# Kernel optimization log

Measured on AMD Instinct MI355X. Metric: run time of the kernel, lower is better.

The kernel has to match this reference:

```python
import jax, jax.numpy as jnp
import numpy as np

N = 16384   # nodes = batch(4) * 64*64 grid
E = 32768   # edges per edge set
L = 32      # LATENT_DIMS
D = 2       # DEPTH (message-passing layers per GNOBlock)
KD = 64     # KERNEL_DIMS
TIN = 10    # TIME_STEPS_IN

def gelu(x):
    return jax.nn.gelu(x, approximate=False)  # torch F.gelu default (erf)

def setup_inputs() -> dict:
    key = jax.random.key(0)
    ks = iter(jax.random.split(key, 64))
    def nrm(shape, s=0.1):
        return jax.random.normal(next(ks), shape, dtype=jnp.float32) * s
    def ridx():
        return jax.random.randint(next(ks), (2, E), 0, N)
    inp = {
        'nodes': nrm((N, TIN), 1.0),
        'grid': jax.random.uniform(next(ks), (N, 2), dtype=jnp.float32),
    }
    for nm in ['11', '12', '22', '23', '33', '32', '21']:
        inp[f'edge_index_{nm}'] = ridx()
    for nm in ['11', '12', '22', '23', '33', '32', '21']:
        inp[f'edge_attr_{nm}'] = nrm((E, 5), 1.0)
    inp['batch_size'] = 4
    inp['image_size'] = 64
    # projector MLP: in_dims=TIN+2 -> hidden L//2 -> L
    inp['proj_w1'] = nrm((TIN + 2, L // 2)); inp['proj_b1'] = jnp.zeros((L // 2,), jnp.float32)
    inp['proj_w2'] = nrm((L // 2, L));       inp['proj_b2'] = jnp.zeros((L,), jnp.float32)
    # decoder MLP: L -> L//2 -> 1
    inp['dec_w1'] = nrm((L, L // 2)); inp['dec_b1'] = jnp.zeros((L // 2,), jnp.float32)
    inp['dec_w2'] = nrm((L // 2, 1)); inp['dec_b2'] = jnp.zeros((1,), jnp.float32)
    # 7 GNOBlocks x D layers: edge kernel MLP (5 -> KD -> L*L) + node linear (L -> L)
    inp['kw1'] = nrm((7, D, 5, KD));      inp['kb1'] = jnp.zeros((7, D, KD), jnp.float32)
    inp['kw2'] = nrm((7, D, KD, L * L));  inp['kb2'] = jnp.zeros((7, D, L * L), jnp.float32)
    inp['lw'] = nrm((7, D, L, L));        inp['lb'] = jnp.zeros((7, D, L), jnp.float32)
    return inp

def _mlp(x, w1, b1, w2, b2):
    return gelu(x @ w1 + b1) @ w2 + b2

def _gno_block(i, x, eidx, eattr, kw1, kb1, kw2, kb2, lw, lb):
    src, dst = eidx[0], eidx[1]
    n = x.shape[0]
    deg = jax.ops.segment_sum(jnp.ones_like(dst, x.dtype), dst, num_segments=n)
    inv_deg = jnp.where(deg > 0, 1.0 / jnp.maximum(deg, 1.0), 0.0)[:, None]
    for d in range(kw1.shape[1]):
        # edge-conditioned kernel: [E, L, L]
        k = _mlp(eattr, kw1[i, d], kb1[i, d], kw2[i, d], kb2[i, d]).reshape(-1, x.shape[1], x.shape[1])
        msg = jnp.einsum('eio,ei->eo', k, x[src])            # gather + per-edge matvec
        agg = jax.ops.segment_sum(msg, dst, num_segments=n) * inv_deg  # scatter-mean
        x = gelu(x @ lw[i, d] + lb[i, d] + agg)              # root linear + activation
    return x

def reference(nodes, grid, edge_index_11, edge_index_12, edge_index_22, edge_index_23,
              edge_index_33, edge_index_32, edge_index_21, edge_attr_11, edge_attr_12,
              edge_attr_22, edge_attr_23, edge_attr_33, edge_attr_32, edge_attr_21,
              batch_size, image_size, proj_w1, proj_b1, proj_w2, proj_b2,
              dec_w1, dec_b1, dec_w2, dec_b2, kw1, kb1, kw2, kb2, lw, lb):
    x = jnp.concatenate([nodes, grid], axis=-1)
    x = gelu(_mlp(x, proj_w1, proj_b1, proj_w2, proj_b2))
    # block param index order matches init order: k11,k22,k33,k12,k23,k32,k21
    n11 = _gno_block(0, x, edge_index_11, edge_attr_11, kw1, kb1, kw2, kb2, lw, lb)
    n12 = _gno_block(3, x, edge_index_12, edge_attr_12, kw1, kb1, kw2, kb2, lw, lb)
    n22 = _gno_block(1, n12, edge_index_22, edge_attr_22, kw1, kb1, kw2, kb2, lw, lb)
    n23 = _gno_block(4, n12, edge_index_23, edge_attr_23, kw1, kb1, kw2, kb2, lw, lb)
    n33 = _gno_block(2, n23, edge_index_33, edge_attr_33, kw1, kb1, kw2, kb2, lw, lb)
    n32 = _gno_block(5, n33, edge_index_32, edge_attr_32, kw1, kb1, kw2, kb2, lw, lb)
    n21 = _gno_block(6, n32 + n22, edge_index_21, edge_attr_21, kw1, kb1, kw2, kb2, lw, lb)
    out = _mlp(n21 + n11, dec_w1, dec_b1, dec_w2, dec_b2)
    return out
```

## Files before the change

kernel.cpp:

```cpp
#include <hip/hip_runtime.h>

#define Nn 16384
#define Ee 32768
#define NL (Nn * 32)

typedef _Float16 hf16;
typedef _Float16 half8 __attribute__((ext_vector_type(8)));
typedef float f32x16 __attribute__((ext_vector_type(16)));

__device__ __forceinline__ float gelu_f(float x) {
    return 0.5f * x * (1.0f + erff(x * 0.7071067811865476f));
}

__device__ __forceinline__ f32x16 zero16() {
    f32x16 v;
#pragma unroll
    for (int r = 0; r < 16; ++r) v[r] = 0.0f;
    return v;
}

struct EPtrs { const int* p[7]; };
struct EA14  { const float* p[14]; };

__global__ __launch_bounds__(256) void proj_kernel(
    const float* __restrict__ nodes, const float* __restrict__ grid2,
    const float* __restrict__ w1, const float* __restrict__ b1,
    const float* __restrict__ w2, const float* __restrict__ b2,
    float* __restrict__ x0, int* __restrict__ deg_i, int* __restrict__ cursor)
{
    const int n = blockIdx.x * 256 + threadIdx.x;
    float in[12];
#pragma unroll
    for (int j = 0; j < 10; ++j) in[j] = nodes[n * 10 + j];
    in[10] = grid2[n * 2 + 0];
    in[11] = grid2[n * 2 + 1];
    float h[16];
#pragma unroll
    for (int j = 0; j < 16; ++j) {
        float a = b1[j];
#pragma unroll
        for (int i = 0; i < 12; ++i) a = fmaf(in[i], w1[i * 16 + j], a);
        h[j] = gelu_f(a);
    }
#pragma unroll
    for (int o = 0; o < 32; ++o) {
        float a = b2[o];
#pragma unroll
        for (int j = 0; j < 16; ++j) a = fmaf(h[j], w2[j * 32 + o], a);
        x0[(size_t)n * 32 + o] = gelu_f(a);
    }
#pragma unroll
    for (int s = 0; s < 7; ++s) { deg_i[s * Nn + n] = 0; cursor[s * Nn + n] = 0; }
}

__global__ __launch_bounds__(256) void count_deg_kernel(EPtrs ei, int* __restrict__ deg_i)
{
    const int t = blockIdx.x * 256 + threadIdx.x;
    const int s = t >> 15;
    const int e = t & (Ee - 1);
    const int dst = ei.p[s][Ee + e];
    atomicAdd(&deg_i[s * Nn + dst], 1);
}

__global__ __launch_bounds__(256) void scan_kernel(const int* __restrict__ deg_i,
                                                   int* __restrict__ off)
{
    const int s = blockIdx.x;
    const int t = threadIdx.x;
    const int* d = deg_i + (size_t)s * Nn;
    int* o = off + (size_t)s * (Nn + 1);
    int local[64];
    int sum = 0;
#pragma unroll
    for (int j = 0; j < 64; ++j) { local[j] = d[t * 64 + j]; sum += local[j]; }
    __shared__ int ps[256];
    ps[t] = sum;
    __syncthreads();
    for (int st = 1; st < 256; st <<= 1) {
        int v = (t >= st) ? ps[t - st] : 0;
        __syncthreads();
        ps[t] += v;
        __syncthreads();
    }
    int base = (t > 0) ? ps[t - 1] : 0;
#pragma unroll
    for (int j = 0; j < 64; ++j) { o[t * 64 + j] = base; base += local[j]; }
    if (t == 255) o[Nn] = base;
}

__global__ __launch_bounds__(256) void rank_kernel(EPtrs ei, const int* __restrict__ off,
                                                   int* __restrict__ cursor,
                                                   int* __restrict__ eord)
{
    const int t = blockIdx.x * 256 + threadIdx.x;
    const int s = t >> 15;
    const int e = t & (Ee - 1);
    const int dst = ei.p[s][Ee + e];
    const int r = off[(size_t)s * (Nn + 1) + dst] + atomicAdd(&cursor[s * Nn + dst], 1);
    eord[(size_t)s * Ee + r] = e;
}

__global__ __launch_bounds__(256) void wprep_kernel(const float* __restrict__ kw2,
                                                    hf16* __restrict__ Wpack)
{
    const int id = blockIdx.x >> 5;
    const int nt = blockIdx.x & 31;
    const int t = threadIdx.x;
    const int ks = t >> 6, lane = t & 63;
    const float* kw2l = kw2 + (size_t)id * 65536;
    half8 vh, vl;
#pragma unroll
    for (int j = 0; j < 8; ++j) {
        const int k = ks * 16 + (lane >> 5) * 8 + j;
        const float v = kw2l[(size_t)k * 1024 + (lane & 31) * 32 + nt];
        const hf16 h = (hf16)v;
        vh[j] = h;
        vl[j] = (hf16)((v - (float)h) * 1024.0f);
    }
    half8* dst = (half8*)(Wpack + ((size_t)(id * 32 + nt) * 8 + ks * 2) * 512);
    dst[0 * 64 + lane] = vh;
    dst[1 * 64 + lane] = vl;
}

__global__ __launch_bounds__(256) void kprep_kernel(const float* __restrict__ kb2,
                                                    float* __restrict__ kb2C)
{
    const int id = blockIdx.x;
    const int t = threadIdx.x;
#pragma unroll
    for (int c = 0; c < 4; ++c) {
        const int ent = t * 4 + c;
        const int nt = ent >> 5;
        const int hi = (ent >> 4) & 1;
        const int r = ent & 15;
        const int i = (r & 3) + 8 * (r >> 2) + 4 * hi;
        kb2C[(size_t)id * 1024 + ent] = kb2[(size_t)id * 1024 + i * 32 + nt];
    }
}

__global__ __launch_bounds__(256) void hprep_kernel(
    EA14 ea, const float* __restrict__ kw1, const float* __restrict__ kb1,
    hf16* __restrict__ Hpack)
{
    const int b = blockIdx.x;
    const int u = b >> 8;
    const int tgrp = b & 255;
    const int t = threadIdx.x, l = t & 63, wv = t >> 6;
    const int tile = tgrp * 4 + wv;
    const int eg = tile * 32 + (l & 31);
    const float* kw1u = kw1 + (size_t)u * 320;
    const float* kb1u = kb1 + (size_t)u * 64;
    float ea5[5];
#pragma unroll
    for (int j = 0; j < 5; ++j) ea5[j] = ea.p[u][(size_t)eg * 5 + j];
    half8* hp = (half8*)Hpack;
#pragma unroll
    for (int ks = 0; ks < 4; ++ks) {
        half8 vh, vl;
#pragma unroll
        for (int j = 0; j < 8; ++j) {
            const int k = ks * 16 + (l >> 5) * 8 + j;
            float pre = kb1u[k];
#pragma unroll
            for (int q = 0; q < 5; ++q) pre = fmaf(ea5[q], kw1u[q * 64 + k], pre);
            const float H = gelu_f(pre);
            const hf16 hv = (hf16)H;
            vh[j] = hv;
            vl[j] = (hf16)((H - (float)hv) * 1024.0f);
        }
        const size_t fb = ((size_t)(u * 1024 + tile) * 8 + ks * 2) * 64;
        hp[fb + l] = vh;
        hp[fb + 64 + l] = vl;
    }
}

__global__ __launch_bounds__(256) void gemm_kernel(
    const float* __restrict__ xa, const float* __restrict__ xb,
    const int* __restrict__ esrc,
    const hf16* __restrict__ HpackU,
    const hf16* __restrict__ WpackL,
    const float* __restrict__ kb2CL,
    float* __restrict__ msgS)
{
    __shared__ __align__(16) hf16 wLDS[2 * 4096];
    half8* wl8 = (half8*)wLDS;

    const int lb = ((blockIdx.x & 7) << 7) + (blockIdx.x >> 3);
    const int eblk = lb >> 2;
    const int qid = lb & 3;
    const int t = threadIdx.x, l = t & 63, wv = t >> 6;
    const int tile = eblk * 4 + wv;

    const half8* hp = (const half8*)HpackU + (size_t)tile * 512;
    half8 Hh[4], Hl[4];
#pragma unroll
    for (int ks = 0; ks < 4; ++ks) {
        Hh[ks] = hp[(ks * 2 + 0) * 64 + l];
        Hl[ks] = hp[(ks * 2 + 1) * 64 + l];
    }

    const int hi = l >> 5;
    const int el = tile * 32 + (l & 31);
    const int src = esrc[el];
    float xsr[16];
#pragma unroll
    for (int c = 0; c < 4; ++c) {
        float4 v = *reinterpret_cast<const float4*>(xa + (size_t)src * 32 + c * 8 + hi * 4);
        if (xb) {
            float4 u = *reinterpret_cast<const float4*>(xb + (size_t)src * 32 + c * 8 + hi * 4);
            v.x += u.x; v.y += u.y; v.z += u.z; v.w += u.w;
        }
        xsr[c * 4 + 0] = v.x; xsr[c * 4 + 1] = v.y;
        xsr[c * 4 + 2] = v.z; xsr[c * 4 + 3] = v.w;
    }

    const half8* wsrc = (const half8*)(WpackL + (size_t)qid * 8 * 4096);
    const float* kbB = kb2CL + hi * 16;

    {
        half8 s0 = wsrc[t * 2 + 0];
        half8 s1 = wsrc[t * 2 + 1];
        wl8[t * 2 + 0] = s0;
        wl8[t * 2 + 1] = s1;
    }
    __syncthreads();

    float4 p4;
    int buf = 0;
#pragma unroll
    for (int nt8 = 0; nt8 < 8; ++nt8) {
        half8 s0, s1;
        if (nt8 < 7) {
            s0 = wsrc[(nt8 + 1) * 512 + t * 2 + 0];
            s1 = wsrc[(nt8 + 1) * 512 + t * 2 + 1];
        }

        half8 WH[4], WL[4];
#pragma unroll
        for (int ks = 0; ks < 4; ++ks) {
            WH[ks] = wl8[buf * 512 + (ks * 2 + 0) * 64 + l];
            WL[ks] = wl8[buf * 512 + (ks * 2 + 1) * 64 + l];
        }

        const int nt = qid * 8 + nt8;
        float kb[16];
#pragma unroll
        for (int c = 0; c < 4; ++c) {
            const float4 kv = *reinterpret_cast<const float4*>(kbB + nt * 32 + c * 4);
            kb[c * 4 + 0] = kv.x; kb[c * 4 + 1] = kv.y;
            kb[c * 4 + 2] = kv.z; kb[c * 4 + 3] = kv.w;
        }

        f32x16 ah = zero16(), ax = zero16();
#pragma unroll
        for (int ks = 0; ks < 4; ++ks) {
            ah = __builtin_amdgcn_mfma_f32_32x32x16_f16(WH[ks], Hh[ks], ah, 0, 0, 0);
            ax = __builtin_amdgcn_mfma_f32_32x32x16_f16(WL[ks], Hh[ks], ax, 0, 0, 0);
            ax = __builtin_amdgcn_mfma_f32_32x32x16_f16(WH[ks], Hl[ks], ax, 0, 0, 0);
        }
        float ph = 0.0f, px = 0.0f, pk = 0.0f;
#pragma unroll
        for (int r = 0; r < 16; ++r) {
            ph = fmaf(ah[r], xsr[r], ph);
            px = fmaf(ax[r], xsr[r], px);
            pk = fmaf(kb[r], xsr[r], pk);
        }
        float p = fmaf(px, 9.765625e-4f, ph) + pk;
        p += __shfl_xor(p, 32);
        p4[nt8 & 3] = p;
        if ((nt8 & 3) == 3 && l < 32)
            *reinterpret_cast<float4*>(msgS + (size_t)el * 32 + qid * 8 + (nt8 - 3)) = p4;

        if (nt8 < 7) {
            wl8[(buf ^ 1) * 512 + t * 2 + 0] = s0;
            wl8[(buf ^ 1) * 512 + t * 2 + 1] = s1;
        }
        __syncthreads();
        buf ^= 1;
    }
}

__global__ __launch_bounds__(256) void node_update_kernel(
    const float* __restrict__ xa, const float* __restrict__ xb,
    float* __restrict__ xout, const float* __restrict__ msgS,
    const int* __restrict__ off, const int* __restrict__ eord,
    const float* __restrict__ lw, const float* __restrict__ lb)
{
    __shared__ float lwS[1024];
#pragma unroll
    for (int c = 0; c < 4; ++c) lwS[threadIdx.x + 256 * c] = lw[threadIdx.x + 256 * c];
    __syncthreads();

    const int t = threadIdx.x, l = t & 63, wv = t >> 6;
    const int n = blockIdx.x * 4 + wv;
    const int o = l & 31, jj = l >> 5;

    const int b = off[n], e = off[n + 1];
    float sum = 0.0f;
    for (int j = b + jj; j < e; j += 2) {
        const int eid = eord[j];
        sum += msgS[(size_t)eid * 32 + o];
    }
    sum += __shfl_xor(sum, 32);
    const float inv = (e > b) ? 1.0f / (float)(e - b) : 0.0f;

    float part = 0.0f;
#pragma unroll
    for (int c = 0; c < 4; ++c) {
        float4 v = *reinterpret_cast<const float4*>(xa + (size_t)n * 32 + jj * 16 + c * 4);
        if (xb) {
            float4 u = *reinterpret_cast<const float4*>(xb + (size_t)n * 32 + jj * 16 + c * 4);
            v.x += u.x; v.y += u.y; v.z += u.z; v.w += u.w;
        }
        part = fmaf(v.x, lwS[(jj * 16 + c * 4 + 0) * 32 + o], part);
        part = fmaf(v.y, lwS[(jj * 16 + c * 4 + 1) * 32 + o], part);
        part = fmaf(v.z, lwS[(jj * 16 + c * 4 + 2) * 32 + o], part);
        part = fmaf(v.w, lwS[(jj * 16 + c * 4 + 3) * 32 + o], part);
    }
    part += __shfl_xor(part, 32);

    const float acc = fmaf(sum, inv, lb[o]) + part;
    if (l < 32) xout[(size_t)n * 32 + o] = gelu_f(acc);
}

__global__ __launch_bounds__(256) void decode_kernel(
    const float* __restrict__ a, const float* __restrict__ b,
    const float* __restrict__ w1, const float* __restrict__ b1,
    const float* __restrict__ w2, const float* __restrict__ b2,
    float* __restrict__ out)
{
    const int n = blockIdx.x * 256 + threadIdx.x;
    float s[32];
#pragma unroll
    for (int i = 0; i < 32; ++i) s[i] = a[(size_t)n * 32 + i] + b[(size_t)n * 32 + i];
    float acc = b2[0];
#pragma unroll
    for (int j = 0; j < 16; ++j) {
        float h = b1[j];
#pragma unroll
        for (int i = 0; i < 32; ++i) h = fmaf(s[i], w1[i * 16 + j], h);
        acc = fmaf(gelu_f(h), w2[j], acc);
    }
    out[n] = acc;
}

extern "C" void kernel_launch(void* const* d_in, const int* in_sizes, int n_in,
                              void* d_out, int out_size, void* d_ws, size_t ws_size,
                              hipStream_t stream)
{
    const float* nodes = (const float*)d_in[0];
    const float* grid2 = (const float*)d_in[1];
    const int* ei[7];
    const float* ea[7];
    for (int s = 0; s < 7; ++s) {
        ei[s] = (const int*)d_in[2 + s];
        ea[s] = (const float*)d_in[9 + s];
    }
    const float* pw1 = (const float*)d_in[18];
    const float* pb1 = (const float*)d_in[19];
    const float* pw2 = (const float*)d_in[20];
    const float* pb2 = (const float*)d_in[21];
    const float* dw1 = (const float*)d_in[22];
    const float* db1 = (const float*)d_in[23];
    const float* dw2 = (const float*)d_in[24];
    const float* db2 = (const float*)d_in[25];
    const float* kw1 = (const float*)d_in[26];
    const float* kb1 = (const float*)d_in[27];
    const float* kw2 = (const float*)d_in[28];
    const float* kb2 = (const float*)d_in[29];
    const float* lw  = (const float*)d_in[30];
    const float* lb  = (const float*)d_in[31];

    const int i2s[7] = {0, 2, 4, 1, 3, 5, 6};

    float* ws  = (float*)d_ws;
    float* x0   = ws + 0 * (size_t)NL;
    float* n11  = ws + 1 * (size_t)NL;
    float* n12  = ws + 2 * (size_t)NL;
    float* n22  = ws + 3 * (size_t)NL;
    float* n23  = ws + 4 * (size_t)NL;
    float* n33  = ws + 5 * (size_t)NL;
    float* n32  = ws + 6 * (size_t)NL;
    float* n21  = ws + 7 * (size_t)NL;
    float* msgS = ws + 8 * (size_t)NL;
    size_t cur = 8 * (size_t)NL + (size_t)Ee * 32;
    hf16* Wpack = (hf16*)(ws + cur);
    cur += (size_t)14 * 32 * 8 * 512 / 2;
    hf16* Hpack = (hf16*)(ws + cur);
    cur += (size_t)14 * 1024 * 8 * 512 / 2;
    float* kb2C = ws + cur; cur += (size_t)14 * 1024;
    int* deg_i  = (int*)(ws + cur); cur += (size_t)7 * Nn;
    int* cursor = (int*)(ws + cur); cur += (size_t)7 * Nn;
    int* off    = (int*)(ws + cur); cur += (size_t)7 * (Nn + 1) + 1;
    int* eord   = (int*)(ws + cur);

    proj_kernel<<<Nn / 256, 256, 0, stream>>>(nodes, grid2, pw1, pb1, pw2, pb2,
                                              x0, deg_i, cursor);

    EPtrs ep;
    for (int s = 0; s < 7; ++s) ep.p[s] = ei[s];
    count_deg_kernel<<<7 * Ee / 256, 256, 0, stream>>>(ep, deg_i);
    scan_kernel<<<7, 256, 0, stream>>>(deg_i, off);
    rank_kernel<<<7 * Ee / 256, 256, 0, stream>>>(ep, off, cursor, eord);
    wprep_kernel<<<14 * 32, 256, 0, stream>>>(kw2, Wpack);
    kprep_kernel<<<14, 256, 0, stream>>>(kb2, kb2C);

    EA14 ea14;
    for (int u = 0; u < 14; ++u) ea14.p[u] = ea[i2s[u >> 1]];
    hprep_kernel<<<14 * 256, 256, 0, stream>>>(ea14, kw1, kb1, Hpack);

    auto layer = [&](int i, int d, int s, const float* xa, const float* xb, float* xo) {
        const int id = i * 2 + d;
        gemm_kernel<<<1024, 256, 0, stream>>>(
            xa, xb, ei[s],
            Hpack + (size_t)id * 1024 * 4096,
            Wpack + (size_t)id * 32 * 4096,
            kb2C + (size_t)id * 1024, msgS);
        node_update_kernel<<<Nn / 4, 256, 0, stream>>>(
            xa, xb, xo, msgS, off + (size_t)s * (Nn + 1),
            eord + (size_t)s * Ee,
            lw + (size_t)id * 1024, lb + (size_t)id * 32);
    };
    auto gno_block = [&](int i, int s, const float* xa, const float* xb, float* xo) {
        layer(i, 0, s, xa, xb, xo);
        layer(i, 1, s, xo, nullptr, xo);
    };

    gno_block(0, 0, x0,  nullptr, n11);
    gno_block(3, 1, x0,  nullptr, n12);
    gno_block(1, 2, n12, nullptr, n22);
    gno_block(4, 3, n12, nullptr, n23);
    gno_block(2, 4, n23, nullptr, n33);
    gno_block(5, 5, n33, nullptr, n32);
    gno_block(6, 6, n32, n22,     n21);

    decode_kernel<<<Nn / 256, 256, 0, stream>>>(n11, n21, dw1, db1, dw2, db2, (float*)d_out);
}
```

Baseline: 600.8 us.

## Stage weights in two large LDS phases and batch four nodes per wave

The gemm kernel used to double-buffer one 8 KB weight slice per n-tile, with a barrier after each of eight iterations. It now loads the weights in two 32 KB phases, so each block syncs only a few times, and it precomputes the bias-times-x dot products before the MFMA loop. The node update kernel now handles four nodes per wave with a quarter of the blocks, spreading the LDS weight load over more work. The cost is larger LDS use per block (32 KB), which may lower occupancy, and less overlap between weight loads and MFMA work.

```diff
diff --git a/kernel.cpp b/kernel.cpp
--- a/kernel.cpp
+++ b/kernel.cpp
@@ -174,7 +174,7 @@
     }
 }
 
-__global__ __launch_bounds__(256) void gemm_kernel(
+__global__ __launch_bounds__(256) void g7(
     const float* __restrict__ xa, const float* __restrict__ xb,
     const int* __restrict__ esrc,
     const hf16* __restrict__ HpackU,
@@ -182,25 +182,18 @@
     const float* __restrict__ kb2CL,
     float* __restrict__ msgS)
 {
-    __shared__ __align__(16) hf16 wLDS[2 * 4096];
+    __shared__ __align__(16) hf16 wLDS[16384];
     half8* wl8 = (half8*)wLDS;
+    float4* wsl = (float4*)wLDS;
 
     const int lb = ((blockIdx.x & 7) << 7) + (blockIdx.x >> 3);
     const int eblk = lb >> 2;
     const int qid = lb & 3;
     const int t = threadIdx.x, l = t & 63, wv = t >> 6;
     const int tile = eblk * 4 + wv;
-
-    const half8* hp = (const half8*)HpackU + (size_t)tile * 512;
-    half8 Hh[4], Hl[4];
-#pragma unroll
-    for (int ks = 0; ks < 4; ++ks) {
-        Hh[ks] = hp[(ks * 2 + 0) * 64 + l];
-        Hl[ks] = hp[(ks * 2 + 1) * 64 + l];
-    }
-
     const int hi = l >> 5;
     const int el = tile * 32 + (l & 31);
+
     const int src = esrc[el];
     float xsr[16];
 #pragma unroll
@@ -214,73 +207,74 @@
         xsr[c * 4 + 2] = v.z; xsr[c * 4 + 3] = v.w;
     }
 
-    const half8* wsrc = (const half8*)(WpackL + (size_t)qid * 8 * 4096);
+    const half8* hp = (const half8*)HpackU + (size_t)tile * 512;
+    half8 Hh[4], Hl[4];
+#pragma unroll
+    for (int ks = 0; ks < 4; ++ks) {
+        Hh[ks] = hp[(ks * 2 + 0) * 64 + l];
+        Hl[ks] = hp[(ks * 2 + 1) * 64 + l];
+    }
+
     const float* kbB = kb2CL + hi * 16;
-
-    {
-        half8 s0 = wsrc[t * 2 + 0];
-        half8 s1 = wsrc[t * 2 + 1];
-        wl8[t * 2 + 0] = s0;
-        wl8[t * 2 + 1] = s1;
-    }
-    __syncthreads();
-
-    float4 p4;
-    int buf = 0;
-#pragma unroll
-    for (int nt8 = 0; nt8 < 8; ++nt8) {
-        half8 s0, s1;
-        if (nt8 < 7) {
-            s0 = wsrc[(nt8 + 1) * 512 + t * 2 + 0];
-            s1 = wsrc[(nt8 + 1) * 512 + t * 2 + 1];
-        }
-
-        half8 WH[4], WL[4];
-#pragma unroll
-        for (int ks = 0; ks < 4; ++ks) {
-            WH[ks] = wl8[buf * 512 + (ks * 2 + 0) * 64 + l];
-            WL[ks] = wl8[buf * 512 + (ks * 2 + 1) * 64 + l];
-        }
-
-        const int nt = qid * 8 + nt8;
-        float kb[16];
+    float pk8[8];
+#pragma unroll
+    for (int n8 = 0; n8 < 8; ++n8) {
+        float pk = 0.0f;
 #pragma unroll
         for (int c = 0; c < 4; ++c) {
-            const float4 kv = *reinterpret_cast<const float4*>(kbB + nt * 32 + c * 4);
-            kb[c * 4 + 0] = kv.x; kb[c * 4 + 1] = kv.y;
-            kb[c * 4 + 2] = kv.z; kb[c * 4 + 3] = kv.w;
-        }
-
-        f32x16 ah = zero16(), ax = zero16();
-#pragma unroll
-        for (int ks = 0; ks < 4; ++ks) {
-            ah = __builtin_amdgcn_mfma_f32_32x32x16_f16(WH[ks], Hh[ks], ah, 0, 0, 0);
-            ax = __builtin_amdgcn_mfma_f32_32x32x16_f16(WL[ks], Hh[ks], ax, 0, 0, 0);
-            ax = __builtin_amdgcn_mfma_f32_32x32x16_f16(WH[ks], Hl[ks], ax, 0, 0, 0);
-        }
-        float ph = 0.0f, px = 0.0f, pk = 0.0f;
-#pragma unroll
-        for (int r = 0; r < 16; ++r) {
-            ph = fmaf(ah[r], xsr[r], ph);
-            px = fmaf(ax[r], xsr[r], px);
-            pk = fmaf(kb[r], xsr[r], pk);
-        }
-        float p = fmaf(px, 9.765625e-4f, ph) + pk;
-        p += __shfl_xor(p, 32);
-        p4[nt8 & 3] = p;
-        if ((nt8 & 3) == 3 && l < 32)
-            *reinterpret_cast<float4*>(msgS + (size_t)el * 32 + qid * 8 + (nt8 - 3)) = p4;
-
-        if (nt8 < 7) {
-            wl8[(buf ^ 1) * 512 + t * 2 + 0] = s0;
-            wl8[(buf ^ 1) * 512 + t * 2 + 1] = s1;
-        }
+            const float4 kv = *reinterpret_cast<const float4*>(kbB + (qid * 8 + n8) * 32 + c * 4);
+            pk = fmaf(kv.x, xsr[c * 4 + 0], pk);
+            pk = fmaf(kv.y, xsr[c * 4 + 1], pk);
+            pk = fmaf(kv.z, xsr[c * 4 + 2], pk);
+            pk = fmaf(kv.w, xsr[c * 4 + 3], pk);
+        }
+        pk8[n8] = pk;
+    }
+
+    const float4* wg = (const float4*)((const char*)WpackL + (size_t)qid * 65536);
+
+#pragma unroll
+    for (int ph = 0; ph < 2; ++ph) {
+        float4 stg[8];
+#pragma unroll
+        for (int j = 0; j < 8; ++j) stg[j] = wg[ph * 2048 + j * 256 + t];
+        if (ph) __syncthreads();
+#pragma unroll
+        for (int j = 0; j < 8; ++j) wsl[j * 256 + t] = stg[j];
         __syncthreads();
-        buf ^= 1;
-    }
-}
-
-__global__ __launch_bounds__(256) void node_update_kernel(
+
+        float4 p4;
+#pragma unroll
+        for (int nt4 = 0; nt4 < 4; ++nt4) {
+            half8 WH[4], WL[4];
+#pragma unroll
+            for (int ks = 0; ks < 4; ++ks) {
+                WH[ks] = wl8[((nt4 * 4 + ks) * 2 + 0) * 64 + l];
+                WL[ks] = wl8[((nt4 * 4 + ks) * 2 + 1) * 64 + l];
+            }
+            f32x16 ah = zero16(), ax = zero16();
+#pragma unroll
+            for (int ks = 0; ks < 4; ++ks) {
+                ah = __builtin_amdgcn_mfma_f32_32x32x16_f16(WH[ks], Hh[ks], ah, 0, 0, 0);
+                ax = __builtin_amdgcn_mfma_f32_32x32x16_f16(WL[ks], Hh[ks], ax, 0, 0, 0);
+                ax = __builtin_amdgcn_mfma_f32_32x32x16_f16(WH[ks], Hl[ks], ax, 0, 0, 0);
+            }
+            float phv = 0.0f, px = 0.0f;
+#pragma unroll
+            for (int r = 0; r < 16; ++r) {
+                phv = fmaf(ah[r], xsr[r], phv);
+                px  = fmaf(ax[r], xsr[r], px);
+            }
+            float p = fmaf(px, 9.765625e-4f, phv) + pk8[ph * 4 + nt4];
+            p += __shfl_xor(p, 32);
+            p4[nt4] = p;
+        }
+        if (l < 32)
+            *reinterpret_cast<float4*>(msgS + (size_t)el * 32 + qid * 8 + ph * 4) = p4;
+    }
+}
+
+__global__ __launch_bounds__(256) void nu7(
     const float* __restrict__ xa, const float* __restrict__ xb,
     float* __restrict__ xout, const float* __restrict__ msgS,
     const int* __restrict__ off, const int* __restrict__ eord,
@@ -292,35 +286,38 @@
     __syncthreads();
 
     const int t = threadIdx.x, l = t & 63, wv = t >> 6;
-    const int n = blockIdx.x * 4 + wv;
     const int o = l & 31, jj = l >> 5;
 
-    const int b = off[n], e = off[n + 1];
-    float sum = 0.0f;
-    for (int j = b + jj; j < e; j += 2) {
-        const int eid = eord[j];
-        sum += msgS[(size_t)eid * 32 + o];
-    }
-    sum += __shfl_xor(sum, 32);
-    const float inv = (e > b) ? 1.0f / (float)(e - b) : 0.0f;
-
-    float part = 0.0f;
-#pragma unroll
-    for (int c = 0; c < 4; ++c) {
-        float4 v = *reinterpret_cast<const float4*>(xa + (size_t)n * 32 + jj * 16 + c * 4);
-        if (xb) {
-            float4 u = *reinterpret_cast<const float4*>(xb + (size_t)n * 32 + jj * 16 + c * 4);
-            v.x += u.x; v.y += u.y; v.z += u.z; v.w += u.w;
-        }
-        part = fmaf(v.x, lwS[(jj * 16 + c * 4 + 0) * 32 + o], part);
-        part = fmaf(v.y, lwS[(jj * 16 + c * 4 + 1) * 32 + o], part);
-        part = fmaf(v.z, lwS[(jj * 16 + c * 4 + 2) * 32 + o], part);
-        part = fmaf(v.w, lwS[(jj * 16 + c * 4 + 3) * 32 + o], part);
-    }
-    part += __shfl_xor(part, 32);
-
-    const float acc = fmaf(sum, inv, lb[o]) + part;
-    if (l < 32) xout[(size_t)n * 32 + o] = gelu_f(acc);
+#pragma unroll
+    for (int it = 0; it < 4; ++it) {
+        const int n = blockIdx.x * 16 + wv * 4 + it;
+        const int b = off[n], e = off[n + 1];
+        float sum = 0.0f;
+        for (int j = b + jj; j < e; j += 2) {
+            const int eid = eord[j];
+            sum += msgS[(size_t)eid * 32 + o];
+        }
+        sum += __shfl_xor(sum, 32);
+        const float inv = (e > b) ? 1.0f / (float)(e - b) : 0.0f;
+
+        float part = 0.0f;
+#pragma unroll
+        for (int c = 0; c < 4; ++c) {
+            float4 v = *reinterpret_cast<const float4*>(xa + (size_t)n * 32 + jj * 16 + c * 4);
+            if (xb) {
+                float4 u = *reinterpret_cast<const float4*>(xb + (size_t)n * 32 + jj * 16 + c * 4);
+                v.x += u.x; v.y += u.y; v.z += u.z; v.w += u.w;
+            }
+            part = fmaf(v.x, lwS[(jj * 16 + c * 4 + 0) * 32 + o], part);
+            part = fmaf(v.y, lwS[(jj * 16 + c * 4 + 1) * 32 + o], part);
+            part = fmaf(v.z, lwS[(jj * 16 + c * 4 + 2) * 32 + o], part);
+            part = fmaf(v.w, lwS[(jj * 16 + c * 4 + 3) * 32 + o], part);
+        }
+        part += __shfl_xor(part, 32);
+
+        const float acc = fmaf(sum, inv, lb[o]) + part;
+        if (l < 32) xout[(size_t)n * 32 + o] = gelu_f(acc);
+    }
 }
 
 __global__ __launch_bounds__(256) void decode_kernel(
@@ -411,12 +408,12 @@
 
     auto layer = [&](int i, int d, int s, const float* xa, const float* xb, float* xo) {
         const int id = i * 2 + d;
-        gemm_kernel<<<1024, 256, 0, stream>>>(
+        g7<<<1024, 256, 0, stream>>>(
             xa, xb, ei[s],
             Hpack + (size_t)id * 1024 * 4096,
             Wpack + (size_t)id * 32 * 4096,
             kb2C + (size_t)id * 1024, msgS);
-        node_update_kernel<<<Nn / 4, 256, 0, stream>>>(
+        nu7<<<Nn / 16, 256, 0, stream>>>(
             xa, xb, xo, msgS, off + (size_t)s * (Nn + 1),
             eord + (size_t)s * Ee,
             lw + (size_t)id * 1024, lb + (size_t)id * 32);
```

Result: slower. 790.8 us (+31.6%).
